# Kernel optimization log

Hardware: AMD Instinct MI355X
Metric: run time of the kernel (lower is better)

## Reference

```python
import jax, jax.numpy as jnp
import numpy as np

B, MAXLEN, Z, HE, HD, K = 512, 128, 128, 512, 2048, 20
NOUT = 6 * K + 3  # sketch-rnn MDN head: 6 params per mixture + 3 pen logits


def _lstm(x, mask, h0, c0, Wih, Whh, b):
    # x: [B,T,D], mask: [B,T] bool; PyTorch gate order i,f,g,o
    xs = jnp.swapaxes(x, 0, 1)          # [T,B,D]
    ms = jnp.swapaxes(mask, 0, 1)[..., None]  # [T,B,1]

    def step(carry, inp):
        h, c = carry
        xt, mt = inp
        g = xt @ Wih.T + h @ Whh.T + b
        i, f, gg, o = jnp.split(g, 4, axis=-1)
        c2 = jax.nn.sigmoid(f) * c + jax.nn.sigmoid(i) * jnp.tanh(gg)
        h2 = jax.nn.sigmoid(o) * jnp.tanh(c2)
        h2 = jnp.where(mt, h2, h)
        c2 = jnp.where(mt, c2, c)
        return (h2, c2), h2

    (hT, cT), hs = jax.lax.scan(step, (h0, c0), (xs, ms))
    return jnp.swapaxes(hs, 0, 1), hT


def setup_inputs() -> dict:
    key = jax.random.key(0)
    ks = jax.random.split(key, 20)

    def w(k, shape, fan):
        return jax.random.normal(k, shape, jnp.float32) / np.sqrt(fan)

    return {
        "data": jax.random.normal(ks[0], (B, MAXLEN + 1, 2), jnp.float32),
        "eps": jax.random.normal(ks[1], (B, Z), jnp.float32),
        "enc_Wih_f": w(ks[2], (4 * HE, 2), 2),
        "enc_Whh_f": w(ks[3], (4 * HE, HE), HE),
        "enc_b_f": jnp.zeros((4 * HE,), jnp.float32),
        "enc_Wih_b": w(ks[4], (4 * HE, 2), 2),
        "enc_Whh_b": w(ks[5], (4 * HE, HE), HE),
        "enc_b_b": jnp.zeros((4 * HE,), jnp.float32),
        "enc_out_W": 0.001 * jax.random.normal(ks[6], (2 * Z, 2 * HE), jnp.float32),
        "enc_out_b": jnp.zeros((2 * Z,), jnp.float32),
        "init_W": 0.001 * jax.random.normal(ks[7], (2 * HD, Z), jnp.float32),
        "init_b": jnp.zeros((2 * HD,), jnp.float32),
        "dec_Wih": w(ks[8], (4 * HD, 5 + Z), 5 + Z),
        "dec_Whh": w(ks[9], (4 * HD, HD), HD),
        "dec_b": jnp.zeros((4 * HD,), jnp.float32),
        "out_W": w(ks[10], (NOUT, HD), HD),
        "out_b": jnp.zeros((NOUT,), jnp.float32),
        "lengths": jax.random.randint(ks[11], (B,), 1, MAXLEN + 2).astype(jnp.int32),
    }


def reference(data, eps, enc_Wih_f, enc_Whh_f, enc_b_f, enc_Wih_b, enc_Whh_b, enc_b_b,
              enc_out_W, enc_out_b, init_W, init_b, dec_Wih, dec_Whh, dec_b,
              out_W, out_b, lengths):
    enc_in = data[:, 1:MAXLEN + 1, :]   # [B,T,2]
    dec_in = data[:, :MAXLEN, :]        # [B,T,2]

    # --- encoder (bidirectional LSTM with length masking == packed seq) ---
    L = jnp.clip(lengths, 1, MAXLEN)
    t = jnp.arange(MAXLEN)
    mask = t[None, :] < L[:, None]      # [B,T]
    z0 = jnp.zeros((B, HE), jnp.float32)
    _, hF = _lstm(enc_in, mask, z0, z0, enc_Wih_f, enc_Whh_f, enc_b_f)
    # reverse each sequence within its valid length for the backward direction
    idx = jnp.clip(L[:, None] - 1 - t[None, :], 0)
    x_rev = jnp.take_along_axis(enc_in, idx[:, :, None], axis=1)
    _, hB = _lstm(x_rev, mask, z0, z0, enc_Wih_b, enc_Whh_b, enc_b_b)
    h_n = jnp.concatenate([hF, hB], axis=-1)          # [B, 2*HE]
    zm, zl = jnp.split(h_n @ enc_out_W.T + enc_out_b, 2, axis=-1)
    z = zm + jnp.exp(0.5 * zl) * eps                  # reparameterize

    # --- decoder init state ---
    h0, c0 = jnp.split(jnp.tanh(z @ init_W.T + init_b), 2, axis=-1)

    # pad stroke channels 2 -> 5, concat z per step
    dec_pad = jnp.pad(dec_in, ((0, 0), (0, 0), (0, 3)))
    dx = jnp.concatenate(
        [dec_pad, jnp.broadcast_to(z[:, None, :], (B, MAXLEN, Z))], axis=-1)

    full_mask = jnp.ones((B, MAXLEN), bool)
    hs, _ = _lstm(dx, full_mask, h0, c0, dec_Wih, dec_Whh, dec_b)  # [B,T,HD]

    params = hs @ out_W.T + out_b  # [B,T,6K+3] mixture-density params
    return (params, zm, zl)
```

## Files before the change

kernel.cpp:

```cpp
#include <hip/hip_runtime.h>
#include <cstddef>
#include <cstdint>

typedef unsigned short u16;

constexpr int B_ = 512, T_ = 128, Z_ = 128, HE_ = 512, HD_ = 2048, NOUT_ = 123;

constexpr size_t OFF_HF   = 0;
constexpr size_t OFF_CF   = OFF_HF + (size_t)B_*HE_;
constexpr size_t OFF_HB   = OFF_CF + (size_t)B_*HE_;
constexpr size_t OFF_CB   = OFF_HB + (size_t)B_*HE_;
constexpr size_t OFF_HD   = OFF_CB + (size_t)B_*HE_;
constexpr size_t OFF_CD   = OFF_HD + (size_t)B_*HD_;
constexpr size_t OFF_ZW   = OFF_CD + (size_t)B_*HD_;
constexpr size_t OFF_G    = OFF_ZW + (size_t)B_*4*HD_;
constexpr size_t OFF_HN   = OFF_G  + (size_t)B_*4*HD_;
constexpr size_t OFF_ZMZL = OFF_HN + (size_t)B_*2*HE_;
constexpr size_t OFF_Z    = OFF_ZMZL + (size_t)B_*2*Z_;
constexpr size_t OFF_WX   = OFF_Z + (size_t)B_*Z_;
constexpr size_t BASE_FLOATS = OFF_WX + (size_t)2*4*HD_;

constexpr size_t SH_WDEC  = 0;
constexpr size_t SH_WENCF = SH_WDEC  + (size_t)4*HD_*HD_;
constexpr size_t SH_WENCB = SH_WENCF + (size_t)4*HE_*HE_;
constexpr size_t SH_OUTW  = SH_WENCB + (size_t)4*HE_*HE_;
constexpr size_t SH_HDEC  = SH_OUTW  + (size_t)128*HD_;
constexpr size_t SH_HENCF = SH_HDEC  + (size_t)B_*HD_;
constexpr size_t SH_HENCB = SH_HENCF + (size_t)B_*HE_;
constexpr size_t SH_HS    = SH_HENCB + (size_t)B_*HE_;
constexpr size_t HS_SHORTS = (size_t)B_*T_*HD_;

__device__ __forceinline__ float sigm(float x) { return 1.f / (1.f + expf(-x)); }

__device__ __forceinline__ u16 f2bf(float x) {
    union { float f; uint32_t u; } v; v.f = x;
    uint32_t r = v.u + 0x7fffu + ((v.u >> 16) & 1u);
    return (u16)(r >> 16);
}

using bf16x8 = __attribute__((ext_vector_type(8))) short;
using f32x4  = __attribute__((ext_vector_type(4))) float;

__device__ __forceinline__ void gldl16(const void* g, void* l) {
    __builtin_amdgcn_global_load_lds(
        (const __attribute__((address_space(1))) unsigned int*)g,
        (__attribute__((address_space(3))) unsigned int*)l, 16, 0, 0);
}

__device__ __forceinline__ void gemm_mfma_body(
    const u16* __restrict__ A, const u16* __restrict__ W,
    const float* __restrict__ bias, float* __restrict__ C,
    int Kd, int lda, int ldw, int ldc, int nmax, int m0, int n0)
{
    __shared__ __align__(16) u16 As[128 * 32];
    __shared__ __align__(16) u16 Ws[128 * 32];
    const int tid = threadIdx.x;
    const int lane = tid & 63;
    const int wave = tid >> 6;
    const int wm = (wave & 1) << 6, wn = (wave >> 1) << 6;
    const int fr = lane & 15, fk = lane >> 4;
    f32x4 acc[4][4] = {};

    const int sr = tid >> 2, sk = (tid & 3) << 3;
    const u16* ga0 = A + (size_t)(m0 + sr) * lda + sk;
    const u16* ga1 = ga0 + (size_t)64 * lda;
    const u16* gw0 = W + (size_t)(n0 + sr) * ldw + sk;
    const u16* gw1 = gw0 + (size_t)64 * ldw;
    u16* la0 = As + tid * 8;
    u16* la1 = la0 + 2048;
    u16* lw0 = Ws + tid * 8;
    u16* lw1 = lw0 + 2048;

    for (int k0 = 0; k0 < Kd; k0 += 32) {
        gldl16(ga0 + k0, la0);
        gldl16(ga1 + k0, la1);
        gldl16(gw0 + k0, lw0);
        gldl16(gw1 + k0, lw1);
        __syncthreads();
        bf16x8 af[4], wf[4];
#pragma unroll
        for (int i = 0; i < 4; ++i)
            af[i] = *reinterpret_cast<const bf16x8*>(&As[(wm + i * 16 + fr) * 32 + fk * 8]);
#pragma unroll
        for (int j = 0; j < 4; ++j)
            wf[j] = *reinterpret_cast<const bf16x8*>(&Ws[(wn + j * 16 + fr) * 32 + fk * 8]);
#pragma unroll
        for (int i = 0; i < 4; ++i)
#pragma unroll
            for (int j = 0; j < 4; ++j)
                acc[i][j] = __builtin_amdgcn_mfma_f32_16x16x32_bf16(af[i], wf[j], acc[i][j], 0, 0, 0);
        __syncthreads();
    }

    const int cr = (lane >> 4) << 2, cc = lane & 15;
#pragma unroll
    for (int j = 0; j < 4; ++j) {
        int n = n0 + wn + j * 16 + cc;
        if (n < nmax) {
            float bv = bias ? bias[n] : 0.f;
#pragma unroll
            for (int i = 0; i < 4; ++i) {
                int m = m0 + wm + i * 16 + cr;
                float* cp = C + (size_t)m * ldc + n;
#pragma unroll
                for (int r = 0; r < 4; ++r)
                    cp[(size_t)r * ldc] = acc[i][j][r] + bv;
            }
        }
    }
}

__global__ __launch_bounds__(256) void gemm_bf16_k(
    const u16* __restrict__ A, const u16* __restrict__ W,
    const float* __restrict__ bias, float* __restrict__ C,
    int Kd, int lda, int ldw, int ldc, int nmax)
{
    gemm_mfma_body(A, W, bias, C, Kd, lda, ldw, ldc, nmax,
                   blockIdx.x * 128, blockIdx.y * 128);
}

__global__ __launch_bounds__(256) void gemm_enc_mfma(
    const u16* __restrict__ hF, const u16* __restrict__ hB,
    const u16* __restrict__ Wf, const u16* __restrict__ Wb,
    float* __restrict__ g)
{
    const u16* A = blockIdx.z ? hB : hF;
    const u16* W = blockIdx.z ? Wb : Wf;
    float* C = g + (size_t)blockIdx.z * ((size_t)B_ * 4 * HE_);
    gemm_mfma_body(A, W, nullptr, C, HE_, HE_, HE_, 4 * HE_, 4 * HE_,
                   blockIdx.x * 128, blockIdx.y * 128);
}

__device__ __forceinline__ void gemm_body(
    const float* __restrict__ A, const float* __restrict__ W,
    const float* __restrict__ bias, float* __restrict__ C,
    int N, int Kd, int lda, int aoff, int ldw, int woff,
    int ldc, int coff, int m0, int n0)
{
    __shared__ __align__(16) float As[16][68];
    __shared__ __align__(16) float Ws[16][68];
    const int tid = threadIdx.x;
    const int tx = tid & 15, ty = tid >> 4;
    float acc[4][4] = {};
    for (int k0 = 0; k0 < Kd; k0 += 16) {
#pragma unroll
        for (int i = 0; i < 4; ++i) {
            int e = tid + i * 256;
            int mm = e >> 4, kk = e & 15;
            As[kk][mm] = A[(size_t)(m0 + mm) * lda + aoff + k0 + kk];
        }
#pragma unroll
        for (int i = 0; i < 4; ++i) {
            int e = tid + i * 256;
            int nn = e >> 4, kk = e & 15;
            int n = n0 + nn;
            Ws[kk][nn] = (n < N) ? W[(size_t)n * ldw + woff + k0 + kk] : 0.f;
        }
        __syncthreads();
#pragma unroll
        for (int kk = 0; kk < 16; ++kk) {
            float4 a = *reinterpret_cast<const float4*>(&As[kk][ty * 4]);
            float4 w = *reinterpret_cast<const float4*>(&Ws[kk][tx * 4]);
            float av[4] = {a.x, a.y, a.z, a.w};
            float wv[4] = {w.x, w.y, w.z, w.w};
#pragma unroll
            for (int i = 0; i < 4; ++i)
#pragma unroll
                for (int j = 0; j < 4; ++j)
                    acc[i][j] = fmaf(av[i], wv[j], acc[i][j]);
        }
        __syncthreads();
    }
#pragma unroll
    for (int i = 0; i < 4; ++i) {
        int m = m0 + ty * 4 + i;
#pragma unroll
        for (int j = 0; j < 4; ++j) {
            int n = n0 + tx * 4 + j;
            if (n < N) {
                float v = acc[i][j];
                if (bias) v += bias[n];
                C[(size_t)m * ldc + coff + n] = v;
            }
        }
    }
}

__global__ __launch_bounds__(256) void gemm_k(
    const float* __restrict__ A, const float* __restrict__ W,
    const float* __restrict__ bias, float* __restrict__ C,
    int N, int Kd, int lda, int aoff, int ldw, int woff, int ldc, int coff)
{
    gemm_body(A, W, bias, C, N, Kd, lda, aoff, ldw, woff, ldc, coff,
              blockIdx.x * 64, blockIdx.y * 64);
}

__global__ __launch_bounds__(256) void conv_bf16(
    const float* __restrict__ src, u16* __restrict__ dst, int n)
{
    int stride = gridDim.x * 256;
    for (int i = blockIdx.x * 256 + threadIdx.x; i < n; i += stride)
        dst[i] = f2bf(src[i]);
}

__global__ __launch_bounds__(256) void conv_outw(
    const float* __restrict__ w, u16* __restrict__ dst)
{
    int i = blockIdx.x * 256 + threadIdx.x;
    int row = i >> 11, col = i & 2047;
    dst[i] = (row < NOUT_) ? f2bf(w[(size_t)row * HD_ + col]) : (u16)0;
}

__global__ __launch_bounds__(256) void point_enc(
    const float* __restrict__ g, const float* __restrict__ data,
    const float* __restrict__ Wih_f, const float* __restrict__ bf,
    const float* __restrict__ Wih_b, const float* __restrict__ bb,
    const int* __restrict__ lengths,
    float* __restrict__ hF, float* __restrict__ cF,
    float* __restrict__ hB, float* __restrict__ cB,
    u16* __restrict__ hFb, u16* __restrict__ hBb, int t)
{
    int idx = blockIdx.x * 256 + threadIdx.x;
    int dir = idx >> 18;
    int r = idx & ((1 << 18) - 1);
    int b = r >> 9, n = r & 511;
    int L = lengths[b]; L = L < 1 ? 1 : (L > 128 ? 128 : L);
    if (t >= L) return;
    const float* gp = g + (size_t)dir * ((size_t)B_ * 4 * HE_) + (size_t)b * (4 * HE_);
    float gi = gp[n], gf = gp[HE_ + n], gg = gp[2 * HE_ + n], go = gp[3 * HE_ + n];
    int row = dir ? (L - 1 - t) : t;
    float x0 = data[b * 258 + (row + 1) * 2 + 0];
    float x1 = data[b * 258 + (row + 1) * 2 + 1];
    const float* Wih = dir ? Wih_b : Wih_f;
    const float* bias = dir ? bb : bf;
    gi += bias[n]          + x0 * Wih[2 * n]              + x1 * Wih[2 * n + 1];
    gf += bias[HE_ + n]    + x0 * Wih[2 * (HE_ + n)]      + x1 * Wih[2 * (HE_ + n) + 1];
    gg += bias[2*HE_ + n]  + x0 * Wih[2 * (2*HE_ + n)]    + x1 * Wih[2 * (2*HE_ + n) + 1];
    go += bias[3*HE_ + n]  + x0 * Wih[2 * (3*HE_ + n)]    + x1 * Wih[2 * (3*HE_ + n) + 1];
    float* h = dir ? hB : hF;
    float* c = dir ? cB : cF;
    u16* hb = dir ? hBb : hFb;
    int o = b * HE_ + n;
    float c2 = sigm(gf) * c[o] + sigm(gi) * tanhf(gg);
    float h2 = sigm(go) * tanhf(c2);
    h[o] = h2; c[o] = c2; hb[o] = f2bf(h2);
}

__global__ __launch_bounds__(256) void copy_hn(
    const float* __restrict__ hF, const float* __restrict__ hB, float* __restrict__ hn)
{
    int i = blockIdx.x * 256 + threadIdx.x;
    int b = i >> 10, j = i & 1023;
    hn[i] = (j < 512) ? hF[b * 512 + j] : hB[b * 512 + j - 512];
}

__global__ __launch_bounds__(256) void point_z(
    const float* __restrict__ zmzl, const float* __restrict__ eps,
    float* __restrict__ ozm, float* __restrict__ ozl, float* __restrict__ z)
{
    int i = blockIdx.x * 256 + threadIdx.x;
    int b = i >> 7, j = i & 127;
    float zm = zmzl[b * 256 + j], zl = zmzl[b * 256 + 128 + j];
    ozm[i] = zm; ozl[i] = zl;
    z[i] = zm + expf(0.5f * zl) * eps[i];
}

__global__ __launch_bounds__(256) void point_init(
    const float* __restrict__ g, float* __restrict__ h, float* __restrict__ c,
    u16* __restrict__ hb)
{
    int i = blockIdx.x * 256 + threadIdx.x;
    int b = i >> 11, n = i & 2047;
    float hv = tanhf(g[(size_t)b * 4096 + n]);
    h[i] = hv; hb[i] = f2bf(hv);
    c[i] = tanhf(g[(size_t)b * 4096 + 2048 + n]);
}

__global__ __launch_bounds__(256) void prep_wx(
    const float* __restrict__ Wih, float* __restrict__ wx)
{
    int j = blockIdx.x * 256 + threadIdx.x;
    wx[j] = Wih[(size_t)j * 133];
    wx[8192 + j] = Wih[(size_t)j * 133 + 1];
}

__global__ __launch_bounds__(256) void point_dec(
    const float* __restrict__ g, const float* __restrict__ zW,
    const float* __restrict__ data, const float* __restrict__ wx,
    float* __restrict__ h, float* __restrict__ c,
    u16* __restrict__ hb, u16* __restrict__ hs, int t)
{
    int idx = blockIdx.x * 256 + threadIdx.x;
    int b = idx >> 11, n = idx & 2047;
    float x0 = data[b * 258 + t * 2 + 0];
    float x1 = data[b * 258 + t * 2 + 1];
    const float* gp = g + (size_t)b * 8192;
    const float* zp = zW + (size_t)b * 8192;
    int j0 = n, j1 = 2048 + n, j2 = 4096 + n, j3 = 6144 + n;
    float gi = gp[j0] + zp[j0] + x0 * wx[j0] + x1 * wx[8192 + j0];
    float gf = gp[j1] + zp[j1] + x0 * wx[j1] + x1 * wx[8192 + j1];
    float gg = gp[j2] + zp[j2] + x0 * wx[j2] + x1 * wx[8192 + j2];
    float go = gp[j3] + zp[j3] + x0 * wx[j3] + x1 * wx[8192 + j3];
    float c2 = sigm(gf) * c[idx] + sigm(gi) * tanhf(gg);
    float h2 = sigm(go) * tanhf(c2);
    h[idx] = h2; c[idx] = c2;
    u16 hv = f2bf(h2);
    hb[idx] = hv;
    if (hs) hs[(size_t)b * (T_ * HD_) + (size_t)t * HD_ + n] = hv;
}

__global__ __launch_bounds__(256) void proj_step(
    const float* __restrict__ h, const float* __restrict__ out_W,
    const float* __restrict__ out_b, float* __restrict__ out, int t)
{
    __shared__ __align__(16) float sh[2048];
    int b = blockIdx.x;
    for (int i = threadIdx.x; i < 2048; i += 256) sh[i] = h[(size_t)b * 2048 + i];
    __syncthreads();
    int n = threadIdx.x >> 1, half = threadIdx.x & 1;
    if (n >= NOUT_) return;
    const float4* w4 = reinterpret_cast<const float4*>(out_W + (size_t)n * 2048 + half * 1024);
    const float4* h4 = reinterpret_cast<const float4*>(sh + half * 1024);
    float s = 0.f;
#pragma unroll 4
    for (int k = 0; k < 256; ++k) {
        float4 a = h4[k], w = w4[k];
        s += a.x * w.x + a.y * w.y + a.z * w.z + a.w * w.w;
    }
    s += __shfl_xor(s, 1);
    if (half == 0) out[(size_t)b * (T_ * NOUT_) + (size_t)t * NOUT_ + n] = s + out_b[n];
}

extern "C" void kernel_launch(void* const* d_in, const int* in_sizes, int n_in,
                              void* d_out, int out_size, void* d_ws, size_t ws_size,
                              hipStream_t stream)
{
    const float* data      = (const float*)d_in[0];
    const float* eps       = (const float*)d_in[1];
    const float* enc_Wih_f = (const float*)d_in[2];
    const float* enc_Whh_f = (const float*)d_in[3];
    const float* enc_b_f   = (const float*)d_in[4];
    const float* enc_Wih_b = (const float*)d_in[5];
    const float* enc_Whh_b = (const float*)d_in[6];
    const float* enc_b_b   = (const float*)d_in[7];
    const float* enc_out_W = (const float*)d_in[8];
    const float* enc_out_b = (const float*)d_in[9];
    const float* init_W    = (const float*)d_in[10];
    const float* init_b    = (const float*)d_in[11];
    const float* dec_Wih   = (const float*)d_in[12];
    const float* dec_Whh   = (const float*)d_in[13];
    const float* dec_b     = (const float*)d_in[14];
    const float* out_W     = (const float*)d_in[15];
    const float* out_b     = (const float*)d_in[16];
    const int*   lengths   = (const int*)d_in[17];

    float* ws  = (float*)d_ws;
    float* out = (float*)d_out;
    float* hF = ws + OFF_HF, *cF = ws + OFF_CF, *hB = ws + OFF_HB, *cB = ws + OFF_CB;
    float* hd = ws + OFF_HD, *cd = ws + OFF_CD;
    float* zW = ws + OFF_ZW, *g = ws + OFF_G, *hn = ws + OFF_HN;
    float* zmzl = ws + OFF_ZMZL, *z = ws + OFF_Z, *wx = ws + OFF_WX;
    u16* bw = (u16*)(ws + BASE_FLOATS);
    u16* wbDec = bw + SH_WDEC, *wbEncF = bw + SH_WENCF, *wbEncB = bw + SH_WENCB;
    u16* wbOut = bw + SH_OUTW;
    u16* hbDec = bw + SH_HDEC, *hbEncF = bw + SH_HENCF, *hbEncB = bw + SH_HENCB;
    float* ozm = out + (size_t)B_ * T_ * NOUT_;
    float* ozl = ozm + (size_t)B_ * Z_;

    conv_bf16<<<4096, 256, 0, stream>>>(dec_Whh, wbDec, 4 * HD_ * HD_);
    conv_bf16<<<1024, 256, 0, stream>>>(enc_Whh_f, wbEncF, 4 * HE_ * HE_);
    conv_bf16<<<1024, 256, 0, stream>>>(enc_Whh_b, wbEncB, 4 * HE_ * HE_);
    conv_outw<<<1024, 256, 0, stream>>>(out_W, wbOut);

    hipMemsetAsync(ws, 0, (size_t)4 * B_ * HE_ * sizeof(float), stream);
    hipMemsetAsync(hbEncF, 0, (size_t)2 * B_ * HE_ * sizeof(u16), stream);

    for (int t = 0; t < T_; ++t) {
        gemm_enc_mfma<<<dim3(4, 16, 2), 256, 0, stream>>>(hbEncF, hbEncB, wbEncF, wbEncB, g);
        point_enc<<<2048, 256, 0, stream>>>(g, data, enc_Wih_f, enc_b_f, enc_Wih_b, enc_b_b,
                                            lengths, hF, cF, hB, cB, hbEncF, hbEncB, t);
    }

    copy_hn<<<2048, 256, 0, stream>>>(hF, hB, hn);
    gemm_k<<<dim3(8, 4), 256, 0, stream>>>(hn, enc_out_W, enc_out_b, zmzl,
                                           256, 1024, 1024, 0, 1024, 0, 256, 0);
    point_z<<<256, 256, 0, stream>>>(zmzl, eps, ozm, ozl, z);
    gemm_k<<<dim3(8, 64), 256, 0, stream>>>(z, init_W, init_b, g,
                                            4096, 128, 128, 0, 128, 0, 4096, 0);
    point_init<<<4096, 256, 0, stream>>>(g, hd, cd, hbDec);
    gemm_k<<<dim3(8, 128), 256, 0, stream>>>(z, dec_Wih, dec_b, zW,
                                             8192, 128, 128, 0, 133, 5, 8192, 0);
    prep_wx<<<32, 256, 0, stream>>>(dec_Wih, wx);

    bool big = ws_size >= BASE_FLOATS * sizeof(float) + (SH_HS + HS_SHORTS) * sizeof(u16);
    u16* hs = big ? (bw + SH_HS) : nullptr;
    for (int t = 0; t < T_; ++t) {
        gemm_bf16_k<<<dim3(4, 64), 256, 0, stream>>>(hbDec, wbDec, nullptr, g,
                                                     2048, 2048, 2048, 8192, 8192);
        point_dec<<<4096, 256, 0, stream>>>(g, zW, data, wx, hd, cd, hbDec, hs, t);
        if (!big) proj_step<<<512, 256, 0, stream>>>(hd, out_W, out_b, out, t);
    }
    if (big) {
        gemm_bf16_k<<<dim3(512, 1), 256, 0, stream>>>(hs, wbOut, out_b, out,
                                                      2048, 2048, 2048, 123, 123);
    }
}
```

Measured before the change: 16.92 ms.

## Fuse LSTM recurrent GEMM with gate pointwise via gate-interleaved weights

Reorders the recurrent weight rows so the four gates of each hidden unit sit next to each other, letting each MFMA output tile hold complete i,f,g,o quadruples. The per-step GEMM and the LSTM cell update are merged into one kernel that gathers the gates with lane shuffles and writes h/c directly, with the bf16 hidden state double-buffered across steps. This removes the fp32 gate buffer round-trip through global memory and one launch per timestep, at the cost of a smaller 64x128 tile and redundant transcendental work on every lane.

```diff
diff --git a/kernel.cpp b/kernel.cpp
--- a/kernel.cpp
+++ b/kernel.cpp
@@ -20,14 +20,17 @@
 constexpr size_t OFF_WX   = OFF_Z + (size_t)B_*Z_;
 constexpr size_t BASE_FLOATS = OFF_WX + (size_t)2*4*HD_;
 
-constexpr size_t SH_WDEC  = 0;
-constexpr size_t SH_WENCF = SH_WDEC  + (size_t)4*HD_*HD_;
-constexpr size_t SH_WENCB = SH_WENCF + (size_t)4*HE_*HE_;
-constexpr size_t SH_OUTW  = SH_WENCB + (size_t)4*HE_*HE_;
-constexpr size_t SH_HDEC  = SH_OUTW  + (size_t)128*HD_;
-constexpr size_t SH_HENCF = SH_HDEC  + (size_t)B_*HD_;
-constexpr size_t SH_HENCB = SH_HENCF + (size_t)B_*HE_;
-constexpr size_t SH_HS    = SH_HENCB + (size_t)B_*HE_;
+constexpr size_t SH_WDEC   = 0;
+constexpr size_t SH_WENCF  = SH_WDEC   + (size_t)4*HD_*HD_;
+constexpr size_t SH_WENCB  = SH_WENCF  + (size_t)4*HE_*HE_;
+constexpr size_t SH_OUTW   = SH_WENCB  + (size_t)4*HE_*HE_;
+constexpr size_t SH_HDEC0  = SH_OUTW   + (size_t)128*HD_;
+constexpr size_t SH_HDEC1  = SH_HDEC0  + (size_t)B_*HD_;
+constexpr size_t SH_HENCF0 = SH_HDEC1  + (size_t)B_*HD_;
+constexpr size_t SH_HENCB0 = SH_HENCF0 + (size_t)B_*HE_;
+constexpr size_t SH_HENCF1 = SH_HENCB0 + (size_t)B_*HE_;
+constexpr size_t SH_HENCB1 = SH_HENCF1 + (size_t)B_*HE_;
+constexpr size_t SH_HS     = SH_HENCB1 + (size_t)B_*HE_;
 constexpr size_t HS_SHORTS = (size_t)B_*T_*HD_;
 
 __device__ __forceinline__ float sigm(float x) { return 1.f / (1.f + expf(-x)); }
@@ -45,6 +48,177 @@
     __builtin_amdgcn_global_load_lds(
         (const __attribute__((address_space(1))) unsigned int*)g,
         (__attribute__((address_space(3))) unsigned int*)l, 16, 0, 0);
+}
+
+__global__ __launch_bounds__(256) void dec_step_fused(
+    const u16* __restrict__ hin, u16* __restrict__ hout,
+    const u16* __restrict__ Wil, const float* __restrict__ zW,
+    const float* __restrict__ data, const float* __restrict__ wx,
+    float* __restrict__ h32, float* __restrict__ c32,
+    u16* __restrict__ hs, int t)
+{
+    __shared__ __align__(16) u16 As[64 * 32];
+    __shared__ __align__(16) u16 Ws[128 * 32];
+    const int tid = threadIdx.x, lane = tid & 63, wave = tid >> 6;
+    const int n0 = blockIdx.x * 128, m0 = blockIdx.y * 64;
+    const int wn = wave << 5;
+    const int fr = lane & 15, fk = lane >> 4;
+    f32x4 acc[4][2] = {};
+
+    const int sr = tid >> 2, sk = (tid & 3) << 3;
+    const u16* ga  = hin + (size_t)(m0 + sr) * 2048 + sk;
+    const u16* gw0 = Wil + (size_t)(n0 + sr) * 2048 + sk;
+    const u16* gw1 = gw0 + (size_t)64 * 2048;
+    u16* la  = As + tid * 8;
+    u16* lw0 = Ws + tid * 8;
+    u16* lw1 = lw0 + 2048;
+
+    for (int k0 = 0; k0 < 2048; k0 += 32) {
+        gldl16(ga + k0, la);
+        gldl16(gw0 + k0, lw0);
+        gldl16(gw1 + k0, lw1);
+        __syncthreads();
+        bf16x8 af[4], wf[2];
+#pragma unroll
+        for (int i = 0; i < 4; ++i)
+            af[i] = *reinterpret_cast<const bf16x8*>(&As[(i * 16 + fr) * 32 + fk * 8]);
+#pragma unroll
+        for (int j = 0; j < 2; ++j)
+            wf[j] = *reinterpret_cast<const bf16x8*>(&Ws[(wn + j * 16 + fr) * 32 + fk * 8]);
+#pragma unroll
+        for (int i = 0; i < 4; ++i)
+#pragma unroll
+            for (int j = 0; j < 2; ++j)
+                acc[i][j] = __builtin_amdgcn_mfma_f32_16x16x32_bf16(af[i], wf[j], acc[i][j], 0, 0, 0);
+        __syncthreads();
+    }
+
+    const int cr = (lane >> 4) << 2, cc = lane & 15;
+    const int gate = cc & 3, lb = lane & ~3;
+#pragma unroll
+    for (int i = 0; i < 4; ++i) {
+#pragma unroll
+        for (int r = 0; r < 4; ++r) {
+            int m = m0 + i * 16 + cr + r;
+            float x0 = data[m * 258 + t * 2 + 0];
+            float x1 = data[m * 258 + t * 2 + 1];
+#pragma unroll
+            for (int j = 0; j < 2; ++j) {
+                int np = n0 + wn + j * 16 + cc;
+                int h = np >> 2;
+                int no = gate * 2048 + h;
+                float v = acc[i][j][r] + zW[(size_t)m * 8192 + no]
+                          + x0 * wx[no] + x1 * wx[8192 + no];
+                float gi = __shfl(v, lb);
+                float gf = __shfl(v, lb | 1);
+                float gg = __shfl(v, lb | 2);
+                float go = __shfl(v, lb | 3);
+                int o = m * 2048 + h;
+                float c2 = sigm(gf) * c32[o] + sigm(gi) * tanhf(gg);
+                float h2 = sigm(go) * tanhf(c2);
+                if (gate == 0) h32[o] = h2;
+                else if (gate == 1) c32[o] = c2;
+                else if (gate == 2) hout[o] = f2bf(h2);
+                else if (hs) hs[(size_t)m * (T_ * HD_) + (size_t)t * HD_ + h] = f2bf(h2);
+            }
+        }
+    }
+}
+
+__global__ __launch_bounds__(256) void enc_step_fused(
+    const u16* __restrict__ hFi, const u16* __restrict__ hBi,
+    u16* __restrict__ hFo, u16* __restrict__ hBo,
+    const u16* __restrict__ WF, const u16* __restrict__ WB,
+    const float* __restrict__ WihF, const float* __restrict__ bF,
+    const float* __restrict__ WihB, const float* __restrict__ bB,
+    const float* __restrict__ data, const int* __restrict__ lengths,
+    float* __restrict__ hF32, float* __restrict__ cF32,
+    float* __restrict__ hB32, float* __restrict__ cB32, int t)
+{
+    __shared__ __align__(16) u16 As[64 * 32];
+    __shared__ __align__(16) u16 Ws[128 * 32];
+    const int dir = blockIdx.z;
+    const u16* A   = dir ? hBi : hFi;
+    const u16* Wm  = dir ? WB : WF;
+    const float* Wih = dir ? WihB : WihF;
+    const float* bia = dir ? bB : bF;
+    const u16* hbi = dir ? hBi : hFi;
+    u16* hbo       = dir ? hBo : hFo;
+    float* h32     = dir ? hB32 : hF32;
+    float* c32     = dir ? cB32 : cF32;
+
+    const int tid = threadIdx.x, lane = tid & 63, wave = tid >> 6;
+    const int n0 = blockIdx.x * 128, m0 = blockIdx.y * 64;
+    const int wn = wave << 5;
+    const int fr = lane & 15, fk = lane >> 4;
+    f32x4 acc[4][2] = {};
+
+    const int sr = tid >> 2, sk = (tid & 3) << 3;
+    const u16* ga  = A  + (size_t)(m0 + sr) * 512 + sk;
+    const u16* gw0 = Wm + (size_t)(n0 + sr) * 512 + sk;
+    const u16* gw1 = gw0 + (size_t)64 * 512;
+    u16* la  = As + tid * 8;
+    u16* lw0 = Ws + tid * 8;
+    u16* lw1 = lw0 + 2048;
+
+    for (int k0 = 0; k0 < 512; k0 += 32) {
+        gldl16(ga + k0, la);
+        gldl16(gw0 + k0, lw0);
+        gldl16(gw1 + k0, lw1);
+        __syncthreads();
+        bf16x8 af[4], wf[2];
+#pragma unroll
+        for (int i = 0; i < 4; ++i)
+            af[i] = *reinterpret_cast<const bf16x8*>(&As[(i * 16 + fr) * 32 + fk * 8]);
+#pragma unroll
+        for (int j = 0; j < 2; ++j)
+            wf[j] = *reinterpret_cast<const bf16x8*>(&Ws[(wn + j * 16 + fr) * 32 + fk * 8]);
+#pragma unroll
+        for (int i = 0; i < 4; ++i)
+#pragma unroll
+            for (int j = 0; j < 2; ++j)
+                acc[i][j] = __builtin_amdgcn_mfma_f32_16x16x32_bf16(af[i], wf[j], acc[i][j], 0, 0, 0);
+        __syncthreads();
+    }
+
+    const int cr = (lane >> 4) << 2, cc = lane & 15;
+    const int gate = cc & 3, lb = lane & ~3;
+#pragma unroll
+    for (int i = 0; i < 4; ++i) {
+#pragma unroll
+        for (int r = 0; r < 4; ++r) {
+            int m = m0 + i * 16 + cr + r;
+            int L = lengths[m]; L = L < 1 ? 1 : (L > 128 ? 128 : L);
+            bool act = (t < L);
+            float x0 = 0.f, x1 = 0.f;
+            if (act) {
+                int row = dir ? (L - 1 - t) : t;
+                x0 = data[m * 258 + (row + 1) * 2 + 0];
+                x1 = data[m * 258 + (row + 1) * 2 + 1];
+            }
+#pragma unroll
+            for (int j = 0; j < 2; ++j) {
+                int np = n0 + wn + j * 16 + cc;
+                int h = np >> 2;
+                int no = gate * 512 + h;
+                float v = acc[i][j][r] + bia[no] + x0 * Wih[2 * no] + x1 * Wih[2 * no + 1];
+                float gi = __shfl(v, lb);
+                float gf = __shfl(v, lb | 1);
+                float gg = __shfl(v, lb | 2);
+                float go = __shfl(v, lb | 3);
+                int o = m * 512 + h;
+                if (act) {
+                    float c2 = sigm(gf) * c32[o] + sigm(gi) * tanhf(gg);
+                    float h2 = sigm(go) * tanhf(c2);
+                    if (gate == 0) h32[o] = h2;
+                    else if (gate == 1) c32[o] = c2;
+                    else if (gate == 2) hbo[o] = f2bf(h2);
+                } else if (gate == 2) {
+                    hbo[o] = hbi[o];
+                }
+            }
+        }
+    }
 }
 
 __device__ __forceinline__ void gemm_mfma_body(
@@ -119,18 +293,6 @@
                    blockIdx.x * 128, blockIdx.y * 128);
 }
 
-__global__ __launch_bounds__(256) void gemm_enc_mfma(
-    const u16* __restrict__ hF, const u16* __restrict__ hB,
-    const u16* __restrict__ Wf, const u16* __restrict__ Wb,
-    float* __restrict__ g)
-{
-    const u16* A = blockIdx.z ? hB : hF;
-    const u16* W = blockIdx.z ? Wb : Wf;
-    float* C = g + (size_t)blockIdx.z * ((size_t)B_ * 4 * HE_);
-    gemm_mfma_body(A, W, nullptr, C, HE_, HE_, HE_, 4 * HE_, 4 * HE_,
-                   blockIdx.x * 128, blockIdx.y * 128);
-}
-
 __device__ __forceinline__ void gemm_body(
     const float* __restrict__ A, const float* __restrict__ W,
     const float* __restrict__ bias, float* __restrict__ C,
@@ -195,12 +357,28 @@
               blockIdx.x * 64, blockIdx.y * 64);
 }
 
-__global__ __launch_bounds__(256) void conv_bf16(
-    const float* __restrict__ src, u16* __restrict__ dst, int n)
-{
-    int stride = gridDim.x * 256;
-    for (int i = blockIdx.x * 256 + threadIdx.x; i < n; i += stride)
-        dst[i] = f2bf(src[i]);
+__global__ __launch_bounds__(256) void conv_wdec_il(
+    const float* __restrict__ src, u16* __restrict__ dst)
+{
+    int row = blockIdx.x;
+    int g = row >> 11, h = row & 2047;
+    size_t so = (size_t)row * 2048, dofs = (size_t)(h * 4 + g) * 2048;
+    for (int k = threadIdx.x; k < 2048; k += 256)
+        dst[dofs + k] = f2bf(src[so + k]);
+}
+
+__global__ __launch_bounds__(256) void conv_wenc_il(
+    const float* __restrict__ srcF, const float* __restrict__ srcB,
+    u16* __restrict__ dstF, u16* __restrict__ dstB)
+{
+    int row = blockIdx.x & 2047;
+    int dir = blockIdx.x >> 11;
+    const float* s = dir ? srcB : srcF;
+    u16* d = dir ? dstB : dstF;
+    int g = row >> 9, h = row & 511;
+    size_t so = (size_t)row * 512, dofs = (size_t)(h * 4 + g) * 512;
+    for (int k = threadIdx.x; k < 512; k += 256)
+        d[dofs + k] = f2bf(s[so + k]);
 }
 
 __global__ __launch_bounds__(256) void conv_outw(
@@ -209,41 +387,6 @@
     int i = blockIdx.x * 256 + threadIdx.x;
     int row = i >> 11, col = i & 2047;
     dst[i] = (row < NOUT_) ? f2bf(w[(size_t)row * HD_ + col]) : (u16)0;
-}
-
-__global__ __launch_bounds__(256) void point_enc(
-    const float* __restrict__ g, const float* __restrict__ data,
-    const float* __restrict__ Wih_f, const float* __restrict__ bf,
-    const float* __restrict__ Wih_b, const float* __restrict__ bb,
-    const int* __restrict__ lengths,
-    float* __restrict__ hF, float* __restrict__ cF,
-    float* __restrict__ hB, float* __restrict__ cB,
-    u16* __restrict__ hFb, u16* __restrict__ hBb, int t)
-{
-    int idx = blockIdx.x * 256 + threadIdx.x;
-    int dir = idx >> 18;
-    int r = idx & ((1 << 18) - 1);
-    int b = r >> 9, n = r & 511;
-    int L = lengths[b]; L = L < 1 ? 1 : (L > 128 ? 128 : L);
-    if (t >= L) return;
-    const float* gp = g + (size_t)dir * ((size_t)B_ * 4 * HE_) + (size_t)b * (4 * HE_);
-    float gi = gp[n], gf = gp[HE_ + n], gg = gp[2 * HE_ + n], go = gp[3 * HE_ + n];
-    int row = dir ? (L - 1 - t) : t;
-    float x0 = data[b * 258 + (row + 1) * 2 + 0];
-    float x1 = data[b * 258 + (row + 1) * 2 + 1];
-    const float* Wih = dir ? Wih_b : Wih_f;
-    const float* bias = dir ? bb : bf;
-    gi += bias[n]          + x0 * Wih[2 * n]              + x1 * Wih[2 * n + 1];
-    gf += bias[HE_ + n]    + x0 * Wih[2 * (HE_ + n)]      + x1 * Wih[2 * (HE_ + n) + 1];
-    gg += bias[2*HE_ + n]  + x0 * Wih[2 * (2*HE_ + n)]    + x1 * Wih[2 * (2*HE_ + n) + 1];
-    go += bias[3*HE_ + n]  + x0 * Wih[2 * (3*HE_ + n)]    + x1 * Wih[2 * (3*HE_ + n) + 1];
-    float* h = dir ? hB : hF;
-    float* c = dir ? cB : cF;
-    u16* hb = dir ? hBb : hFb;
-    int o = b * HE_ + n;
-    float c2 = sigm(gf) * c[o] + sigm(gi) * tanhf(gg);
-    float h2 = sigm(go) * tanhf(c2);
-    h[o] = h2; c[o] = c2; hb[o] = f2bf(h2);
 }
 
 __global__ __launch_bounds__(256) void copy_hn(
@@ -282,31 +425,6 @@
     int j = blockIdx.x * 256 + threadIdx.x;
     wx[j] = Wih[(size_t)j * 133];
     wx[8192 + j] = Wih[(size_t)j * 133 + 1];
-}
-
-__global__ __launch_bounds__(256) void point_dec(
-    const float* __restrict__ g, const float* __restrict__ zW,
-    const float* __restrict__ data, const float* __restrict__ wx,
-    float* __restrict__ h, float* __restrict__ c,
-    u16* __restrict__ hb, u16* __restrict__ hs, int t)
-{
-    int idx = blockIdx.x * 256 + threadIdx.x;
-    int b = idx >> 11, n = idx & 2047;
-    float x0 = data[b * 258 + t * 2 + 0];
-    float x1 = data[b * 258 + t * 2 + 1];
-    const float* gp = g + (size_t)b * 8192;
-    const float* zp = zW + (size_t)b * 8192;
-    int j0 = n, j1 = 2048 + n, j2 = 4096 + n, j3 = 6144 + n;
-    float gi = gp[j0] + zp[j0] + x0 * wx[j0] + x1 * wx[8192 + j0];
-    float gf = gp[j1] + zp[j1] + x0 * wx[j1] + x1 * wx[8192 + j1];
-    float gg = gp[j2] + zp[j2] + x0 * wx[j2] + x1 * wx[8192 + j2];
-    float go = gp[j3] + zp[j3] + x0 * wx[j3] + x1 * wx[8192 + j3];
-    float c2 = sigm(gf) * c[idx] + sigm(gi) * tanhf(gg);
-    float h2 = sigm(go) * tanhf(c2);
-    h[idx] = h2; c[idx] = c2;
-    u16 hv = f2bf(h2);
-    hb[idx] = hv;
-    if (hs) hs[(size_t)b * (T_ * HD_) + (size_t)t * HD_ + n] = hv;
 }
 
 __global__ __launch_bounds__(256) void proj_step(
@@ -361,24 +479,30 @@
     float* zW = ws + OFF_ZW, *g = ws + OFF_G, *hn = ws + OFF_HN;
     float* zmzl = ws + OFF_ZMZL, *z = ws + OFF_Z, *wx = ws + OFF_WX;
     u16* bw = (u16*)(ws + BASE_FLOATS);
-    u16* wbDec = bw + SH_WDEC, *wbEncF = bw + SH_WENCF, *wbEncB = bw + SH_WENCB;
-    u16* wbOut = bw + SH_OUTW;
-    u16* hbDec = bw + SH_HDEC, *hbEncF = bw + SH_HENCF, *hbEncB = bw + SH_HENCB;
+    u16* wbDec  = bw + SH_WDEC, *wbEncF = bw + SH_WENCF, *wbEncB = bw + SH_WENCB;
+    u16* wbOut  = bw + SH_OUTW;
+    u16* hD0 = bw + SH_HDEC0,  *hD1 = bw + SH_HDEC1;
+    u16* hEF0 = bw + SH_HENCF0, *hEB0 = bw + SH_HENCB0;
+    u16* hEF1 = bw + SH_HENCF1, *hEB1 = bw + SH_HENCB1;
     float* ozm = out + (size_t)B_ * T_ * NOUT_;
     float* ozl = ozm + (size_t)B_ * Z_;
 
-    conv_bf16<<<4096, 256, 0, stream>>>(dec_Whh, wbDec, 4 * HD_ * HD_);
-    conv_bf16<<<1024, 256, 0, stream>>>(enc_Whh_f, wbEncF, 4 * HE_ * HE_);
-    conv_bf16<<<1024, 256, 0, stream>>>(enc_Whh_b, wbEncB, 4 * HE_ * HE_);
+    conv_wdec_il<<<8192, 256, 0, stream>>>(dec_Whh, wbDec);
+    conv_wenc_il<<<4096, 256, 0, stream>>>(enc_Whh_f, enc_Whh_b, wbEncF, wbEncB);
     conv_outw<<<1024, 256, 0, stream>>>(out_W, wbOut);
 
     hipMemsetAsync(ws, 0, (size_t)4 * B_ * HE_ * sizeof(float), stream);
-    hipMemsetAsync(hbEncF, 0, (size_t)2 * B_ * HE_ * sizeof(u16), stream);
+    hipMemsetAsync(hEF0, 0, (size_t)2 * B_ * HE_ * sizeof(u16), stream);
 
     for (int t = 0; t < T_; ++t) {
-        gemm_enc_mfma<<<dim3(4, 16, 2), 256, 0, stream>>>(hbEncF, hbEncB, wbEncF, wbEncB, g);
-        point_enc<<<2048, 256, 0, stream>>>(g, data, enc_Wih_f, enc_b_f, enc_Wih_b, enc_b_b,
-                                            lengths, hF, cF, hB, cB, hbEncF, hbEncB, t);
+        const u16* fi = (t & 1) ? hEF1 : hEF0;
+        const u16* bi = (t & 1) ? hEB1 : hEB0;
+        u16* fo = (t & 1) ? hEF0 : hEF1;
+        u16* bo = (t & 1) ? hEB0 : hEB1;
+        enc_step_fused<<<dim3(16, 8, 2), 256, 0, stream>>>(
+            fi, bi, fo, bo, wbEncF, wbEncB,
+            enc_Wih_f, enc_b_f, enc_Wih_b, enc_b_b,
+            data, lengths, hF, cF, hB, cB, t);
     }
 
     copy_hn<<<2048, 256, 0, stream>>>(hF, hB, hn);
@@ -387,7 +511,7 @@
     point_z<<<256, 256, 0, stream>>>(zmzl, eps, ozm, ozl, z);
     gemm_k<<<dim3(8, 64), 256, 0, stream>>>(z, init_W, init_b, g,
                                             4096, 128, 128, 0, 128, 0, 4096, 0);
-    point_init<<<4096, 256, 0, stream>>>(g, hd, cd, hbDec);
+    point_init<<<4096, 256, 0, stream>>>(g, hd, cd, hD0);
     gemm_k<<<dim3(8, 128), 256, 0, stream>>>(z, dec_Wih, dec_b, zW,
                                              8192, 128, 128, 0, 133, 5, 8192, 0);
     prep_wx<<<32, 256, 0, stream>>>(dec_Wih, wx);
@@ -395,9 +519,10 @@
     bool big = ws_size >= BASE_FLOATS * sizeof(float) + (SH_HS + HS_SHORTS) * sizeof(u16);
     u16* hs = big ? (bw + SH_HS) : nullptr;
     for (int t = 0; t < T_; ++t) {
-        gemm_bf16_k<<<dim3(4, 64), 256, 0, stream>>>(hbDec, wbDec, nullptr, g,
-                                                     2048, 2048, 2048, 8192, 8192);
-        point_dec<<<4096, 256, 0, stream>>>(g, zW, data, wx, hd, cd, hbDec, hs, t);
+        const u16* hi = (t & 1) ? hD1 : hD0;
+        u16* ho = (t & 1) ? hD0 : hD1;
+        dec_step_fused<<<dim3(64, 8), 256, 0, stream>>>(
+            hi, ho, wbDec, zW, data, wx, hd, cd, hs, t);
         if (!big) proj_step<<<512, 256, 0, stream>>>(hd, out_W, out_b, out, t);
     }
     if (big) {
```

Result: slower. 19.08 ms (+12.8%).
